# Optimization experiments

Measured on AMD Instinct MI355X. Metric: run time of the kernel, lower is better.

## Reference

```python
import jax, jax.numpy as jnp
import numpy as np

NUM_HEADS = 12
SEQ_H = 32
SEQ_W = 32
D_HALF = 32
ROPE_BASE = 10000.0
LN_EPS = 1e-5


def build_rope_cache(seq_len, head_dim, base=ROPE_BASE):
    inv_freq = 1.0 / base ** (jnp.arange(0, head_dim, 2, dtype=jnp.float32) / head_dim)
    t = jnp.arange(seq_len, dtype=jnp.float32)
    freqs = jnp.outer(t, inv_freq)  # [seq_len, head_dim//2]
    cos = jnp.repeat(jnp.cos(freqs), 2, axis=-1)  # [seq_len, head_dim]
    sin = jnp.repeat(jnp.sin(freqs), 2, axis=-1)
    return cos, sin


def apply_rope(x, cos, sin):
    # x: [B,H,N,d_sub], cos/sin: [N,d_sub]
    x_even, x_odd = x[..., ::2], x[..., 1::2]
    x_rot = jnp.stack([-x_odd, x_even], axis=-1).reshape(x.shape)
    return x * cos[None, None] + x_rot * sin[None, None]


def setup_inputs() -> dict:
    key = jax.random.key(0)
    ks = jax.random.split(key, 3)
    B, N, D = 8, 1025, 768
    return {
        "x": jax.random.normal(ks[0], (B, N, D), dtype=jnp.float32),
        "ln_g": jnp.ones((D,), dtype=jnp.float32),
        "ln_b": jnp.zeros((D,), dtype=jnp.float32),
        "w_qkv": jax.random.normal(ks[1], (3 * D, D), dtype=jnp.float32) * 0.02,
        "w_proj": jax.random.normal(ks[2], (D, D), dtype=jnp.float32) * 0.02,
        "b_proj": jnp.zeros((D,), dtype=jnp.float32),
    }


def reference(x, ln_g, ln_b, w_qkv, w_proj, b_proj):
    B, N, D = x.shape
    H = NUM_HEADS
    hd = D // H
    d2 = D_HALF
    scale = hd ** -0.5

    # LayerNorm
    mu = jnp.mean(x, axis=-1, keepdims=True)
    var = jnp.mean(jnp.square(x - mu), axis=-1, keepdims=True)
    xn = (x - mu) * jax.lax.rsqrt(var + LN_EPS) * ln_g + ln_b

    # QKV projection (no bias)
    qkv = jnp.einsum("bnd,ed->bne", xn, w_qkv).reshape(B, N, 3, H, hd)
    qkv = jnp.transpose(qkv, (2, 0, 3, 1, 4))  # [3,B,H,N,hd]
    q, k, v = qkv[0], qkv[1], qkv[2]

    # 2D position ids (CLS token -> row 0, col 0)
    patch_lin = jnp.arange(N - 1)
    rows = patch_lin // SEQ_W
    cols = patch_lin % SEQ_W
    zero = jnp.zeros((1,), dtype=patch_lin.dtype)
    row_ids = jnp.concatenate([zero, rows])
    col_ids = jnp.concatenate([zero, cols])

    cos_row, sin_row = build_rope_cache(SEQ_H, d2)
    cos_col, sin_col = build_rope_cache(SEQ_W, d2)
    cos_r, sin_r = cos_row[row_ids], sin_row[row_ids]  # [N,d2]
    cos_c, sin_c = cos_col[col_ids], sin_col[col_ids]

    q = jnp.concatenate(
        [apply_rope(q[..., :d2], cos_r, sin_r), apply_rope(q[..., d2:], cos_c, sin_c)], axis=-1)
    k = jnp.concatenate(
        [apply_rope(k[..., :d2], cos_r, sin_r), apply_rope(k[..., d2:], cos_c, sin_c)], axis=-1)

    attn = jnp.einsum("bhqd,bhkd->bhqk", q, k) * scale
    attn = jax.nn.softmax(attn, axis=-1)
    out = jnp.einsum("bhqk,bhkd->bhqd", attn, v)  # [B,H,N,hd]
    out = jnp.transpose(out, (0, 2, 1, 3)).reshape(B, N, D)
    return jnp.einsum("bnd,ed->bne", out, w_proj) + b_proj
```

## Files before the change

### kernel.cpp

```cpp
#include <hip/hip_runtime.h>
#include <hip/hip_bf16.h>

typedef unsigned short u16;

#define B_      8
#define N_      1025
#define D_      768
#define H_      12
#define HD_     64
#define M_REAL  (B_ * N_)
#define M_PAD   8320
#define QKVC    (3 * D_)
#define LN_BLK  (M_REAL / 4)

typedef __attribute__((ext_vector_type(8))) short bf16x8;
typedef __attribute__((ext_vector_type(4))) float f32x4;

static __device__ __forceinline__ float bf2f(u16 u) {
    union { unsigned int i; float f; } v; v.i = ((unsigned int)u) << 16; return v.f;
}
static __device__ __forceinline__ u16 f2bf(float f) {
    union { float f; unsigned int i; } v; v.f = f;
    unsigned int x = v.i;
    return (u16)((x + 0x7fffu + ((x >> 16) & 1u)) >> 16);
}
static __device__ __forceinline__ unsigned int cvtpk(float a, float b) {
    unsigned int r;
    asm volatile("v_cvt_pk_bf16_f32 %0, %1, %2" : "=v"(r) : "v"(a), "v"(b));
    return r;
}

static __device__ __forceinline__ void g2l16(const u16* g, u16* l) {
    __builtin_amdgcn_global_load_lds(
        (const __attribute__((address_space(1))) unsigned int*)g,
        (__attribute__((address_space(3))) unsigned int*)l, 16, 0, 0);
}

__global__ __launch_bounds__(256)
void ln_f2b_kernel(const float* __restrict__ x, const float* __restrict__ g,
                   const float* __restrict__ bvec, u16* __restrict__ xn,
                   const float* __restrict__ wq, u16* __restrict__ wqb,
                   const float* __restrict__ wp, u16* __restrict__ wpb)
{
    const int tid = threadIdx.x;
    if (blockIdx.x >= LN_BLK) {
        int i = (blockIdx.x - LN_BLK) * 1024 + tid * 4;
        const float* src; u16* dst;
        if (i < QKVC * D_) { src = wq + i; dst = wqb + i; }
        else { src = wp + (i - QKVC * D_); dst = wpb + (i - QKVC * D_); }
        float4 v = *(const float4*)src;
        dst[0] = f2bf(v.x); dst[1] = f2bf(v.y);
        dst[2] = f2bf(v.z); dst[3] = f2bf(v.w);
        return;
    }
    const int wave = tid >> 6, lane = tid & 63;
    const int row  = blockIdx.x * 4 + wave;
    const float* xr = x + (size_t)row * D_;
    float4 v[3];
    float s = 0.f, ss = 0.f;
#pragma unroll
    for (int j = 0; j < 3; j++) {
        float4 t = *(const float4*)&xr[j * 256 + lane * 4];
        v[j] = t;
        s  += (t.x + t.y) + (t.z + t.w);
        ss += (t.x * t.x + t.y * t.y) + (t.z * t.z + t.w * t.w);
    }
#pragma unroll
    for (int off = 1; off < 64; off <<= 1) {
        s  += __shfl_xor(s,  off);
        ss += __shfl_xor(ss, off);
    }
    const float mean = s * (1.0f / D_);
    const float var  = ss * (1.0f / D_) - mean * mean;
    const float rs   = rsqrtf(var + 1e-5f);
    u16* outr = xn + (size_t)row * D_;
#pragma unroll
    for (int j = 0; j < 3; j++) {
        int c = j * 256 + lane * 4;
        float4 g4 = *(const float4*)&g[c];
        float4 b4 = *(const float4*)&bvec[c];
        u16 o[4];
        o[0] = f2bf((v[j].x - mean) * rs * g4.x + b4.x);
        o[1] = f2bf((v[j].y - mean) * rs * g4.y + b4.y);
        o[2] = f2bf((v[j].z - mean) * rs * g4.z + b4.z);
        o[3] = f2bf((v[j].w - mean) * rs * g4.w + b4.w);
        *(uint2*)&outr[c] = *(const uint2*)o;
    }
}

template <typename OutT, bool ROPE>
__global__ __launch_bounds__(256)
void gemm_bt(const u16* __restrict__ A, const u16* __restrict__ B,
             OutT* __restrict__ C, const float* __restrict__ bias,
             int M_real, int Ncols, int K,
             int BM, int BN, int gh, int gw, int PC)
{
    const int l   = blockIdx.x;
    const int xcd = l & 7;
    const int i0  = l >> 3;
    const int pr  = xcd / PC, pc = xcd % PC;
    const int bm  = pr * gh + (i0 % gh);
    const int bn  = pc * gw + (i0 / gh);
    if (bm >= BM || bn >= BN) return;

    __shared__ __align__(16) unsigned char smem[34816];
    u16* As0 = (u16*)smem;
    u16* Bs0 = (u16*)(smem + 8192);
    u16*   ep16 = (u16*)smem;
    float* ep32 = (float*)smem;

    const int tid  = threadIdx.x;
    const int wave = tid >> 6, lane = tid & 63;
    const int wm   = (wave >> 1) * 64, wn = (wave & 1) * 64;
    const int lrow = lane & 15, lq = lane >> 4;
    const int lrow4 = lane >> 2, lchunk = lane & 3;

    int ar0 = bm * 128 + wave * 16 + lrow4;       if (ar0 >= M_real) ar0 = M_real - 1;
    int ar1 = bm * 128 + (wave + 4) * 16 + lrow4; if (ar1 >= M_real) ar1 = M_real - 1;
    const u16* apg0 = A + (size_t)ar0 * K + lchunk * 8;
    const u16* apg1 = A + (size_t)ar1 * K + lchunk * 8;
    const u16* bpg0 = B + (size_t)(bn * 128 + wave * 16 + lrow4) * K + lchunk * 8;
    const u16* bpg1 = B + (size_t)(bn * 128 + (wave + 4) * 16 + lrow4) * K + lchunk * 8;
    u16* asl0 = As0 + wave * 512;       u16* asl1 = As0 + (wave + 4) * 512;
    u16* bsl0 = Bs0 + wave * 512;       u16* bsl1 = Bs0 + (wave + 4) * 512;
    const int bufoff = 8192;

    f32x4 acc[4][4];
#pragma unroll
    for (int i = 0; i < 4; i++)
#pragma unroll
        for (int j = 0; j < 4; j++)
            acc[i][j] = (f32x4){0.f, 0.f, 0.f, 0.f};

    g2l16(apg0, asl0); g2l16(apg1, asl1);
    g2l16(bpg0, bsl0); g2l16(bpg1, bsl1);

    const int kTiles = K / 32;
    for (int kt = 0; kt < kTiles; kt++) {
        const int cur = kt & 1;
        if (kt + 1 < kTiles) {
            const int k1 = (kt + 1) * 32;
            const int no = (cur ^ 1) * bufoff;
            g2l16(apg0 + k1, asl0 + no); g2l16(apg1 + k1, asl1 + no);
            g2l16(bpg0 + k1, bsl0 + no); g2l16(bpg1 + k1, bsl1 + no);
            asm volatile("s_waitcnt vmcnt(4)" ::: "memory");
        } else {
            asm volatile("s_waitcnt vmcnt(0)" ::: "memory");
        }
        __builtin_amdgcn_s_barrier();

        const u16* Asr = As0 + cur * bufoff;
        const u16* Bsr = Bs0 + cur * bufoff;
        bf16x8 af[4], bfr[4];
#pragma unroll
        for (int i = 0; i < 4; i++) {
            af[i]  = *(const bf16x8*)&Asr[(wm + i * 16 + lrow) * 32 + lq * 8];
            bfr[i] = *(const bf16x8*)&Bsr[(wn + i * 16 + lrow) * 32 + lq * 8];
        }
        __builtin_amdgcn_s_setprio(1);
#pragma unroll
        for (int i = 0; i < 4; i++)
#pragma unroll
            for (int j = 0; j < 4; j++)
                acc[i][j] = __builtin_amdgcn_mfma_f32_16x16x32_bf16(af[i], bfr[j], acc[i][j], 0, 0, 0);
        __builtin_amdgcn_s_setprio(0);
        __builtin_amdgcn_s_barrier();
    }
    __syncthreads();

    if constexpr (sizeof(OutT) == 2) {
#pragma unroll
        for (int j = 0; j < 4; j++) {
            int gcol = bn * 128 + wn + j * 16 + lrow;
            float bv = bias ? bias[gcol] : 0.f;
            int qk = gcol / D_;
            int dh = gcol & 63;
            int half = dh >> 5, ii = (dh & 31) >> 1;
            float sgn = (dh & 1) ? 1.f : -1.f;
            float invf = exp2f(-(float)ii * 0.8304820237218406f);
#pragma unroll
            for (int i = 0; i < 4; i++)
#pragma unroll
                for (int r = 0; r < 4; r++) {
                    int grow = bm * 128 + wm + i * 16 + lq * 4 + r;
                    float val = acc[i][j][r] + bv;
                    if constexpr (ROPE) {
                        if (qk < 2) {
                            float partner = __shfl_xor(val, 1);
                            int n = grow % N_;
                            int pl = n - 1;
                            int pos = (n == 0) ? 0 : (half ? (pl & 31) : (pl >> 5));
                            float ang = (float)pos * invf;
                            val = val * __cosf(ang) + sgn * partner * __sinf(ang);
                            if (qk == 0) val *= 0.125f;
                        }
                    }
                    ep16[(wm + i * 16 + lq * 4 + r) * 136 + wn + j * 16 + lrow] = f2bf(val);
                }
        }
        __syncthreads();
#pragma unroll
        for (int c = 0; c < 8; c++) {
            int idx = tid + c * 256;
            int row = idx >> 4, l16 = idx & 15;
            int grow = bm * 128 + row;
            if (grow < M_real)
                *(uint4*)((u16*)C + (size_t)grow * Ncols + bn * 128 + l16 * 8) =
                    *(const uint4*)&ep16[row * 136 + l16 * 8];
        }
    } else {
#pragma unroll
        for (int s = 0; s < 2; s++) {
            if (s) __syncthreads();
            if (wm == s * 64) {
#pragma unroll
                for (int j = 0; j < 4; j++) {
                    int gcol = bn * 128 + wn + j * 16 + lrow;
                    float bv = bias ? bias[gcol] : 0.f;
#pragma unroll
                    for (int i = 0; i < 4; i++)
#pragma unroll
                        for (int r = 0; r < 4; r++)
                            ep32[(i * 16 + lq * 4 + r) * 132 + wn + j * 16 + lrow] =
                                acc[i][j][r] + bv;
                }
            }
            __syncthreads();
#pragma unroll
            for (int c = 0; c < 8; c++) {
                int idx = tid + c * 256;
                int row = idx >> 5, l32 = idx & 31;
                int grow = bm * 128 + s * 64 + row;
                if (grow < M_real)
                    *(uint4*)((float*)C + (size_t)grow * Ncols + bn * 128 + l32 * 4) =
                        *(const uint4*)&ep32[row * 132 + l32 * 4];
            }
        }
    }
}

__global__ __launch_bounds__(256)
void attn_mfma(const u16* __restrict__ qkv, u16* __restrict__ out)
{
    __shared__ __align__(16) u16 Kt[2][64][72];
    __shared__ __align__(16) u16 Vt[2][64][72];
    __shared__ float Lw[4][32];

    const int l   = blockIdx.x;
    const int xcd = l & 7;
    const int j0  = l >> 3;
    const int bh  = xcd * 12 + j0 / 9;
    const int b  = bh / H_, h = bh % H_;
    const int q0 = (j0 % 9) * 128;
    const int tid  = threadIdx.x;
    const int wave = tid >> 6, lane = tid & 63;
    const int lm = lane & 15, lq = lane >> 4;
    const int qw = q0 + wave * 32;

    const int vcol = (lane & 35) | ((lane & 12) << 1) | ((lane & 16) >> 2);

    bf16x8 qf[2][2];
#pragma unroll
    for (int sq = 0; sq < 2; sq++) {
        int qrow = qw + sq * 16 + lm; if (qrow > N_ - 1) qrow = N_ - 1;
        const u16* qptr = qkv + (size_t)(b * N_ + qrow) * QKVC + h * HD_;
        qf[sq][0] = *(const bf16x8*)(qptr + lq * 8);
        qf[sq][1] = *(const bf16x8*)(qptr + 32 + lq * 8);
    }

    float l_r[2] = {0.f, 0.f};
    f32x4 o_acc[2][4];
#pragma unroll
    for (int sq = 0; sq < 2; sq++)
#pragma unroll
        for (int t = 0; t < 4; t++)
            o_acc[sq][t] = (f32x4){0.f, 0.f, 0.f, 0.f};

    bf16x8 kreg[2], vreg[2];
    {
        int krow = lane; if (krow > N_ - 1) krow = N_ - 1;
        const u16* kvp = qkv + (size_t)(b * N_ + krow) * QKVC + h * HD_;
#pragma unroll
        for (int p = 0; p < 2; p++) {
            int dg = wave + p * 4;
            kreg[p] = *(const bf16x8*)(kvp + D_ + dg * 8);
            vreg[p] = *(const bf16x8*)(kvp + 2 * D_ + dg * 8);
        }
    }

    const int kTiles = (N_ + 63) / 64;
    for (int kt = 0; kt < kTiles; kt++) {
        const int kbase = kt * 64;
        const int buf = kt & 1;

#pragma unroll
        for (int pp = 0; pp < 2; pp++) {
            int dg = wave + pp * 4;
            *(bf16x8*)&Kt[buf][lane][dg * 8] = kreg[pp];
#pragma unroll
            for (int j = 0; j < 8; j++)
                Vt[buf][dg * 8 + j][vcol] = (u16)vreg[pp][j];
        }

        if (kt + 1 < kTiles) {
            int krow = kbase + 64 + lane; if (krow > N_ - 1) krow = N_ - 1;
            const u16* kvp = qkv + (size_t)(b * N_ + krow) * QKVC + h * HD_;
#pragma unroll
            for (int pp = 0; pp < 2; pp++) {
                int dg = wave + pp * 4;
                kreg[pp] = *(const bf16x8*)(kvp + D_ + dg * 8);
                vreg[pp] = *(const bf16x8*)(kvp + 2 * D_ + dg * 8);
            }
        }

        asm volatile("s_waitcnt lgkmcnt(0)" ::: "memory");
        __builtin_amdgcn_s_barrier();

        f32x4 sc[2][4];
        __builtin_amdgcn_s_setprio(1);
#pragma unroll
        for (int st = 0; st < 4; st++) {
            bf16x8 kf0 = *(const bf16x8*)&Kt[buf][st * 16 + lm][lq * 8];
            bf16x8 kf1 = *(const bf16x8*)&Kt[buf][st * 16 + lm][32 + lq * 8];
#pragma unroll
            for (int sq = 0; sq < 2; sq++) {
                f32x4 s4 = (f32x4){0.f, 0.f, 0.f, 0.f};
                s4 = __builtin_amdgcn_mfma_f32_16x16x32_bf16(kf0, qf[sq][0], s4, 0, 0, 0);
                s4 = __builtin_amdgcn_mfma_f32_16x16x32_bf16(kf1, qf[sq][1], s4, 0, 0, 0);
                sc[sq][st] = s4;
            }
        }
        __builtin_amdgcn_s_setprio(0);

        const bool lastT = (kt == kTiles - 1);
        bf16x8 pa[2][2];
#pragma unroll
        for (int sq = 0; sq < 2; sq++) {
            union { bf16x8 v; unsigned int u[4]; } pk0, pk1;
#pragma unroll
            for (int st = 0; st < 4; st++) {
                float p0 = __expf(sc[sq][st][0]);
                float p1 = __expf(sc[sq][st][1]);
                float p2 = __expf(sc[sq][st][2]);
                float p3 = __expf(sc[sq][st][3]);
                if (lastT) {
                    const int keyb = kbase + st * 16 + lq * 4;
                    if (keyb + 0 >= N_) p0 = 0.f;
                    if (keyb + 1 >= N_) p1 = 0.f;
                    if (keyb + 2 >= N_) p2 = 0.f;
                    if (keyb + 3 >= N_) p3 = 0.f;
                }
                l_r[sq] += (p0 + p1) + (p2 + p3);
                unsigned int lo = cvtpk(p0, p1);
                unsigned int hi = cvtpk(p2, p3);
                if      (st == 0) { pk0.u[0] = lo; pk0.u[1] = hi; }
                else if (st == 1) { pk0.u[2] = lo; pk0.u[3] = hi; }
                else if (st == 2) { pk1.u[0] = lo; pk1.u[1] = hi; }
                else              { pk1.u[2] = lo; pk1.u[3] = hi; }
            }
            pa[sq][0] = pk0.v; pa[sq][1] = pk1.v;
        }

        __builtin_amdgcn_s_setprio(1);
#pragma unroll
        for (int nt = 0; nt < 4; nt++) {
            bf16x8 vb0 = *(const bf16x8*)&Vt[buf][nt * 16 + lm][lq * 8];
            bf16x8 vb1 = *(const bf16x8*)&Vt[buf][nt * 16 + lm][32 + lq * 8];
#pragma unroll
            for (int sq = 0; sq < 2; sq++) {
                o_acc[sq][nt] = __builtin_amdgcn_mfma_f32_16x16x32_bf16(pa[sq][0], vb0, o_acc[sq][nt], 0, 0, 0);
                o_acc[sq][nt] = __builtin_amdgcn_mfma_f32_16x16x32_bf16(pa[sq][1], vb1, o_acc[sq][nt], 0, 0, 0);
            }
        }
        __builtin_amdgcn_s_setprio(0);
    }

#pragma unroll
    for (int sq = 0; sq < 2; sq++) {
        float l2 = l_r[sq];
        l2 += __shfl_xor(l2, 16);
        l2 += __shfl_xor(l2, 32);
        if (lq == 0) Lw[wave][sq * 16 + lm] = l2;
    }
    asm volatile("s_waitcnt lgkmcnt(0)" ::: "memory");

#pragma unroll
    for (int sq = 0; sq < 2; sq++)
#pragma unroll
        for (int r = 0; r < 4; r++) {
            int q = qw + sq * 16 + lq * 4 + r;
            if (q < N_) {
                float inv = 1.0f / Lw[wave][sq * 16 + lq * 4 + r];
                u16* orow = out + (size_t)(b * N_ + q) * D_ + h * HD_ + lm;
#pragma unroll
                for (int nt = 0; nt < 4; nt++)
                    orow[nt * 16] = f2bf(o_acc[sq][nt][r] * inv);
            }
        }
}

extern "C" void kernel_launch(void* const* d_in, const int* in_sizes, int n_in,
                              void* d_out, int out_size, void* d_ws, size_t ws_size,
                              hipStream_t stream)
{
    const float* x      = (const float*)d_in[0];
    const float* ln_g   = (const float*)d_in[1];
    const float* ln_b   = (const float*)d_in[2];
    const float* w_qkv  = (const float*)d_in[3];
    const float* w_proj = (const float*)d_in[4];
    const float* b_proj = (const float*)d_in[5];

    u16* wqkv_b  = (u16*)d_ws;
    u16* wproj_b = wqkv_b + (size_t)QKVC * D_;
    u16* xn      = wproj_b + (size_t)D_ * D_;
    u16* qkv     = xn + (size_t)M_PAD * D_;
    u16* attno   = xn;

    ln_f2b_kernel<<<LN_BLK + (QKVC * D_ + D_ * D_) / 1024, 256, 0, stream>>>(
        x, ln_g, ln_b, xn, w_qkv, wqkv_b, w_proj, wproj_b);

    gemm_bt<u16, true><<<1224, 256, 0, stream>>>(
        xn, wqkv_b, qkv, nullptr, M_REAL, QKVC, D_,
        65, 18, 17, 9, 2);

    attn_mfma<<<864, 256, 0, stream>>>(qkv, attno);

    gemm_bt<float, false><<<432, 256, 0, stream>>>(
        attno, wproj_b, (float*)d_out, b_proj, M_REAL, D_, D_,
        65, 6, 9, 6, 1);
}
```

Baseline: 211.8 us.

## Load K tiles directly to LDS with XOR swizzle, drop padding

K tiles are now fetched with direct global-to-LDS 16-byte loads (g2l16) into an unpadded, XOR-swizzled layout instead of being staged through registers. V keeps register staging but is stored with an XOR swizzle. The row-sum normalisation uses a lane shuffle instead of an LDS scratch array, and launch bounds now request 5 blocks per CU. The goal is to cut VGPR pressure, LDS footprint and bank conflicts. The cost is that the barrier must now also wait on vmcnt, which exposes some global-load latency.

```diff
diff --git a/kernel.cpp b/kernel.cpp
--- a/kernel.cpp
+++ b/kernel.cpp
@@ -239,12 +239,11 @@
     }
 }
 
-__global__ __launch_bounds__(256)
+__global__ __launch_bounds__(256, 5)
 void attn_mfma(const u16* __restrict__ qkv, u16* __restrict__ out)
 {
-    __shared__ __align__(16) u16 Kt[2][64][72];
-    __shared__ __align__(16) u16 Vt[2][64][72];
-    __shared__ float Lw[4][32];
+    __shared__ __align__(16) u16 Kt[2][64][64];
+    __shared__ __align__(16) u16 Vt[2][64][64];
 
     const int l   = blockIdx.x;
     const int xcd = l & 7;
@@ -259,6 +258,9 @@
 
     const int vcol = (lane & 35) | ((lane & 12) << 1) | ((lane & 16) >> 2);
 
+    const int krlane = lane >> 3;
+    const int kclane = (lane & 7) ^ krlane;
+
     bf16x8 qf[2][2];
 #pragma unroll
     for (int sq = 0; sq < 2; sq++) {
@@ -268,6 +270,9 @@
         qf[sq][1] = *(const bf16x8*)(qptr + 32 + lq * 8);
     }
 
+    const u16* kgb = qkv + (size_t)b * N_ * QKVC + D_ + h * HD_;
+    const u16* vgb = qkv + (size_t)b * N_ * QKVC + 2 * D_ + h * HD_ + wave * 8;
+
     float l_r[2] = {0.f, 0.f};
     f32x4 o_acc[2][4];
 #pragma unroll
@@ -276,16 +281,17 @@
         for (int t = 0; t < 4; t++)
             o_acc[sq][t] = (f32x4){0.f, 0.f, 0.f, 0.f};
 
-    bf16x8 kreg[2], vreg[2];
+    bf16x8 vreg[2];
     {
-        int krow = lane; if (krow > N_ - 1) krow = N_ - 1;
-        const u16* kvp = qkv + (size_t)(b * N_ + krow) * QKVC + h * HD_;
-#pragma unroll
-        for (int p = 0; p < 2; p++) {
-            int dg = wave + p * 4;
-            kreg[p] = *(const bf16x8*)(kvp + D_ + dg * 8);
-            vreg[p] = *(const bf16x8*)(kvp + 2 * D_ + dg * 8);
-        }
+#pragma unroll
+        for (int i = 0; i < 2; i++) {
+            int key = wave * 16 + i * 8 + krlane; if (key > N_ - 1) key = N_ - 1;
+            g2l16(kgb + (size_t)key * QKVC + kclane * 8, &Kt[0][wave * 16 + i * 8][0]);
+        }
+        int vr = lane; if (vr > N_ - 1) vr = N_ - 1;
+        const u16* p = vgb + (size_t)vr * QKVC;
+        vreg[0] = *(const bf16x8*)p;
+        vreg[1] = *(const bf16x8*)(p + 32);
     }
 
     const int kTiles = (N_ + 63) / 64;
@@ -296,32 +302,35 @@
 #pragma unroll
         for (int pp = 0; pp < 2; pp++) {
             int dg = wave + pp * 4;
-            *(bf16x8*)&Kt[buf][lane][dg * 8] = kreg[pp];
 #pragma unroll
             for (int j = 0; j < 8; j++)
-                Vt[buf][dg * 8 + j][vcol] = (u16)vreg[pp][j];
-        }
+                Vt[buf][dg * 8 + j][vcol ^ (j << 3)] = (u16)vreg[pp][j];
+        }
+
+        asm volatile("s_waitcnt vmcnt(0) lgkmcnt(0)" ::: "memory");
+        __builtin_amdgcn_s_barrier();
 
         if (kt + 1 < kTiles) {
-            int krow = kbase + 64 + lane; if (krow > N_ - 1) krow = N_ - 1;
-            const u16* kvp = qkv + (size_t)(b * N_ + krow) * QKVC + h * HD_;
-#pragma unroll
-            for (int pp = 0; pp < 2; pp++) {
-                int dg = wave + pp * 4;
-                kreg[pp] = *(const bf16x8*)(kvp + D_ + dg * 8);
-                vreg[pp] = *(const bf16x8*)(kvp + 2 * D_ + dg * 8);
-            }
-        }
-
-        asm volatile("s_waitcnt lgkmcnt(0)" ::: "memory");
-        __builtin_amdgcn_s_barrier();
+            const int kb = kbase + 64;
+#pragma unroll
+            for (int i = 0; i < 2; i++) {
+                int key = kb + wave * 16 + i * 8 + krlane; if (key > N_ - 1) key = N_ - 1;
+                g2l16(kgb + (size_t)key * QKVC + kclane * 8, &Kt[buf ^ 1][wave * 16 + i * 8][0]);
+            }
+            int vr = kb + lane; if (vr > N_ - 1) vr = N_ - 1;
+            const u16* p = vgb + (size_t)vr * QKVC;
+            vreg[0] = *(const bf16x8*)p;
+            vreg[1] = *(const bf16x8*)(p + 32);
+        }
 
         f32x4 sc[2][4];
         __builtin_amdgcn_s_setprio(1);
 #pragma unroll
         for (int st = 0; st < 4; st++) {
-            bf16x8 kf0 = *(const bf16x8*)&Kt[buf][st * 16 + lm][lq * 8];
-            bf16x8 kf1 = *(const bf16x8*)&Kt[buf][st * 16 + lm][32 + lq * 8];
+            const int krow = st * 16 + lm;
+            const int c0 = lq ^ (krow & 7);
+            bf16x8 kf0 = *(const bf16x8*)&Kt[buf][krow][c0 * 8];
+            bf16x8 kf1 = *(const bf16x8*)&Kt[buf][krow][(c0 ^ 4) * 8];
 #pragma unroll
             for (int sq = 0; sq < 2; sq++) {
                 f32x4 s4 = (f32x4){0.f, 0.f, 0.f, 0.f};
@@ -364,8 +373,10 @@
         __builtin_amdgcn_s_setprio(1);
 #pragma unroll
         for (int nt = 0; nt < 4; nt++) {
-            bf16x8 vb0 = *(const bf16x8*)&Vt[buf][nt * 16 + lm][lq * 8];
-            bf16x8 vb1 = *(const bf16x8*)&Vt[buf][nt * 16 + lm][32 + lq * 8];
+            const int vrow = nt * 16 + lm;
+            const int d0 = lq ^ (vrow & 7);
+            bf16x8 vb0 = *(const bf16x8*)&Vt[buf][vrow][d0 * 8];
+            bf16x8 vb1 = *(const bf16x8*)&Vt[buf][vrow][(d0 ^ 4) * 8];
 #pragma unroll
             for (int sq = 0; sq < 2; sq++) {
                 o_acc[sq][nt] = __builtin_amdgcn_mfma_f32_16x16x32_bf16(pa[sq][0], vb0, o_acc[sq][nt], 0, 0, 0);
@@ -375,14 +386,14 @@
         __builtin_amdgcn_s_setprio(0);
     }
 
+    float lfull[2];
 #pragma unroll
     for (int sq = 0; sq < 2; sq++) {
         float l2 = l_r[sq];
         l2 += __shfl_xor(l2, 16);
         l2 += __shfl_xor(l2, 32);
-        if (lq == 0) Lw[wave][sq * 16 + lm] = l2;
-    }
-    asm volatile("s_waitcnt lgkmcnt(0)" ::: "memory");
+        lfull[sq] = l2;
+    }
 
 #pragma unroll
     for (int sq = 0; sq < 2; sq++)
@@ -390,7 +401,7 @@
         for (int r = 0; r < 4; r++) {
             int q = qw + sq * 16 + lq * 4 + r;
             if (q < N_) {
-                float inv = 1.0f / Lw[wave][sq * 16 + lq * 4 + r];
+                float inv = 1.0f / __shfl(lfull[sq], lq * 4 + r);
                 u16* orow = out + (size_t)(b * N_ + q) * D_ + h * HD_ + lm;
 #pragma unroll
                 for (int nt = 0; nt < 4; nt++)
```

Measured after the change: 289.2 us. +36.5%, slower.
